# Kernel tuning notes

Measured on AMD Instinct MI355X. Metric: run time of the kernel, lower is better.

Reference implementation:

```python
import jax, jax.numpy as jnp
import numpy as np

N_NODES = 50000
N_EDGES = 800000
BATCH = 8
IN_CH = 64
OUT_CH = 64
K = 6


def setup_inputs() -> dict:
    key = jax.random.key(0)
    k1, k2, k3, k4 = jax.random.split(key, 4)
    x = jax.random.normal(k1, (BATCH, N_NODES, IN_CH), dtype=jnp.float32)
    edge_index = jax.random.randint(k2, (2, N_EDGES), 0, N_NODES, dtype=jnp.int64)
    # small weights keep the order-K Chebyshev recursion numerically stable
    edge_weight = jax.random.normal(k3, (N_EDGES,), dtype=jnp.float32) * 0.05
    W = jax.random.normal(k4, (K, IN_CH, OUT_CH), dtype=jnp.float32) * (1.0 / np.sqrt(IN_CH))
    bias = jnp.zeros((OUT_CH,), dtype=jnp.float32)
    return {"x": x, "edge_index": edge_index, "edge_weight": edge_weight, "W": W, "bias": bias}


def _spmm(edge_index, edge_weight, x, n_nodes):
    # sparse Laplacian @ x for batched features x: [B, N, C]
    src = edge_index[1]  # gather column
    dst = edge_index[0]  # scatter row
    msg = x[:, src, :] * edge_weight[None, :, None]      # [B, E, C]
    agg = jax.ops.segment_sum(msg.transpose(1, 0, 2), dst, num_segments=n_nodes)  # [N, B, C]
    return agg.transpose(1, 0, 2)                        # [B, N, C]


def reference(x, edge_index, edge_weight, W, bias):
    n = x.shape[1]
    t_prev = x                                            # T_0
    out = jnp.einsum('bnc,co->bno', t_prev, W[0])
    if K > 1:
        t_cur = _spmm(edge_index, edge_weight, x, n)      # T_1 = L x
        out = out + jnp.einsum('bnc,co->bno', t_cur, W[1])
        for k in range(2, K):
            t_next = 2.0 * _spmm(edge_index, edge_weight, t_cur, n) - t_prev
            out = out + jnp.einsum('bnc,co->bno', t_next, W[k])
            t_prev, t_cur = t_cur, t_next
    out = out + bias
    return out
```

## Files before the change

kernel.cpp:

```cpp
#include <hip/hip_runtime.h>

#define N_NODES 50000
#define N_EDGES 800000
#define BATCH 8
#define CH 64
#define BC (BATCH * CH)
#define WSZ (CH * CH)
#define NROWS (BATCH * N_NODES)
#define TELEMS ((size_t)NROWS * CH)
#define HIST_BLOCKS ((N_EDGES + 255) / 256)
#define CAST_BLOCKS ((int)(TELEMS / 4 / 256))
#define PACK_BLOCKS 12

typedef unsigned short u16;
typedef short bf16x8 __attribute__((ext_vector_type(8)));
typedef float f32x4 __attribute__((ext_vector_type(4)));
typedef unsigned short u16x4 __attribute__((ext_vector_type(4)));
typedef unsigned short u16x8 __attribute__((ext_vector_type(8)));

__device__ __forceinline__ u16 f2bf(float f) {
    unsigned x = __float_as_uint(f);
    return (u16)((x + 0x7fffu + ((x >> 16) & 1u)) >> 16);
}
__device__ __forceinline__ float b2f(u16 u) {
    return __uint_as_float(((unsigned)u) << 16);
}


__global__ __launch_bounds__(256) void hist_cast_kernel(
        const int* __restrict__ dst, int* __restrict__ cursor,
        const float* __restrict__ x, u16* __restrict__ xb) {
    int bid = blockIdx.x;
    if (bid < HIST_BLOCKS) {
        int e = bid * 256 + threadIdx.x;
        if (e < N_EDGES) atomicAdd(&cursor[dst[e]], 1);
        return;
    }
    size_t i = (size_t)(bid - HIST_BLOCKS) * 256 + threadIdx.x;
    f32x4 v = __builtin_nontemporal_load((const f32x4*)(x + i * 4));
    int c4 = (int)(i & 15);
    size_t bn = i >> 4;
    int b = (int)(bn / N_NODES);
    int n = (int)(bn - (size_t)b * N_NODES);
    u16x4 o;
    o.x = f2bf(v.x); o.y = f2bf(v.y); o.z = f2bf(v.z); o.w = f2bf(v.w);
    *(u16x4*)(xb + ((size_t)n * BATCH + b) * CH + c4 * 4) = o;
}

__global__ void scan_kernel(int* cursor, int* __restrict__ row_ptr, int n) {
    const int T = 1024;
    int tid = threadIdx.x;
    int per = (n + T - 1) / T;
    int s = tid * per;
    int e = s + per; if (e > n) e = n;
    int sum = 0;
    for (int i = s; i < e; ++i) sum += cursor[i];
    __shared__ int lds[1024];
    lds[tid] = sum;
    __syncthreads();
    for (int off = 1; off < 1024; off <<= 1) {
        int t = (tid >= off) ? lds[tid - off] : 0;
        __syncthreads();
        lds[tid] += t;
        __syncthreads();
    }
    int run = lds[tid] - sum;
    for (int i = s; i < e; ++i) {
        int v = cursor[i];
        row_ptr[i] = run;
        cursor[i]  = run;
        run += v;
    }
    if (tid == T - 1) row_ptr[n] = run;
}

__global__ __launch_bounds__(256) void scatter_pack_kernel(
        const int* __restrict__ dst, const int* __restrict__ src,
        const float* __restrict__ w, int* cursor, int2* __restrict__ edges,
        const float* __restrict__ W, u16* __restrict__ wpack) {
    int bid = blockIdx.x;
    if (bid < HIST_BLOCKS) {
        int e = bid * 256 + threadIdx.x;
        if (e >= N_EDGES) return;
        int d = dst[e];
        int p = atomicAdd(&cursor[d], 1);
        edges[p] = make_int2(src[e], __float_as_int(w[e]));
        return;
    }
    int id = (bid - HIST_BLOCKS) * 256 + threadIdx.x;
    if (id >= 48 * 64) return;
    int lane = id & 63, frag = id >> 6;
    int ct = frag & 3, cct = (frag >> 2) & 1, k = frag >> 3;
    int m = lane & 15, quad = lane >> 4;
    int c = ct * 16 + m;
#pragma unroll
    for (int j = 0; j < 8; ++j) {
        int cc = cct * 32 + quad * 8 + j;
        wpack[(size_t)id * 8 + j] = f2bf(W[k * WSZ + cc * CH + c]);
    }
}

template <bool HAS_PREV>
__global__ __launch_bounds__(256) void spmm_kernel(
        const u16* __restrict__ tcur,
        const u16* __restrict__ tprev,
        u16* __restrict__ tnext,
        const int* __restrict__ row_ptr,
        const int2* __restrict__ edges,
        int half) {
    const int node = blockIdx.x * 4 + (threadIdx.x >> 6);
    const int lane = threadIdx.x & 63;
    const size_t lo = (size_t)half * 256 + (size_t)lane * 4;

    float acc[4];
#pragma unroll
    for (int q = 0; q < 4; ++q) acc[q] = 0.f;

    const int beg = row_ptr[node], end = row_ptr[node + 1];
    for (int e0 = beg; e0 < end; e0 += 64) {
        int m = end - e0; if (m > 64) m = 64;
        int2 ev = edges[e0 + (lane < m ? lane : 0)];
        int j = 0;
        for (; j + 4 <= m; j += 4) {
            int   s0 = __shfl(ev.x, j);
            int   s1 = __shfl(ev.x, j + 1);
            int   s2 = __shfl(ev.x, j + 2);
            int   s3 = __shfl(ev.x, j + 3);
            float w0 = __int_as_float(__shfl(ev.y, j));
            float w1 = __int_as_float(__shfl(ev.y, j + 1));
            float w2 = __int_as_float(__shfl(ev.y, j + 2));
            float w3 = __int_as_float(__shfl(ev.y, j + 3));
            u16x4 v0 = *(const u16x4*)(tcur + (size_t)s0 * BC + lo);
            u16x4 v1 = *(const u16x4*)(tcur + (size_t)s1 * BC + lo);
            u16x4 v2 = *(const u16x4*)(tcur + (size_t)s2 * BC + lo);
            u16x4 v3 = *(const u16x4*)(tcur + (size_t)s3 * BC + lo);
#pragma unroll
            for (int q = 0; q < 4; ++q) acc[q] = fmaf(w0, b2f(v0[q]), acc[q]);
#pragma unroll
            for (int q = 0; q < 4; ++q) acc[q] = fmaf(w1, b2f(v1[q]), acc[q]);
#pragma unroll
            for (int q = 0; q < 4; ++q) acc[q] = fmaf(w2, b2f(v2[q]), acc[q]);
#pragma unroll
            for (int q = 0; q < 4; ++q) acc[q] = fmaf(w3, b2f(v3[q]), acc[q]);
        }
        for (; j < m; ++j) {
            int   s = __shfl(ev.x, j);
            float w = __int_as_float(__shfl(ev.y, j));
            u16x4 v = *(const u16x4*)(tcur + (size_t)s * BC + lo);
#pragma unroll
            for (int q = 0; q < 4; ++q) acc[q] = fmaf(w, b2f(v[q]), acc[q]);
        }
    }

    const size_t idx = (size_t)node * BC + lo;
    u16x4 o;
    if (HAS_PREV) {
        u16x4 pv = *(const u16x4*)(tprev + idx);
#pragma unroll
        for (int q = 0; q < 4; ++q) o[q] = f2bf(2.f * acc[q] - b2f(pv[q]));
    } else {
#pragma unroll
        for (int q = 0; q < 4; ++q) o[q] = f2bf(acc[q]);
    }
    *(u16x4*)(tnext + idx) = o;
}

template <int NK, bool ACCUM>
__global__ __launch_bounds__(256) void out_gemm(
        const u16* __restrict__ tbase, size_t tstride,
        const u16* __restrict__ wpack,
        const float* __restrict__ bias,
        float* __restrict__ out) {
    const int wave = threadIdx.x >> 6, lane = threadIdx.x & 63;
    const int tile = blockIdx.x * 4 + wave;
    const int row0 = tile * 16;
    const int m = lane & 15, quad = lane >> 4;

    bf16x8 A[NK][2];
#pragma unroll
    for (int k = 0; k < NK; ++k) {
        const u16* t = tbase + (size_t)k * tstride + (size_t)(row0 + m) * CH + quad * 8;
#pragma unroll
        for (int cct = 0; cct < 2; ++cct)
            A[k][cct] = *(const bf16x8*)(t + cct * 32);
    }

    f32x4 acc[4];
#pragma unroll
    for (int ct = 0; ct < 4; ++ct) acc[ct] = (f32x4){0.f, 0.f, 0.f, 0.f};

#pragma unroll
    for (int k = 0; k < NK; ++k) {
#pragma unroll
        for (int cct = 0; cct < 2; ++cct) {
#pragma unroll
            for (int ct = 0; ct < 4; ++ct) {
                bf16x8 B = *(const bf16x8*)(wpack + (size_t)(((k * 2 + cct) * 4 + ct) * 64 + lane) * 8);
                acc[ct] = __builtin_amdgcn_mfma_f32_16x16x32_bf16(A[k][cct], B, acc[ct], 0, 0, 0);
            }
        }
    }

#pragma unroll
    for (int ct = 0; ct < 4; ++ct) {
        const int c = ct * 16 + m;
        const float bv = bias[c];
#pragma unroll
        for (int r = 0; r < 4; ++r) {
            int row = row0 + quad * 4 + r;
            float* op = out + ((size_t)(row & 7) * N_NODES + (row >> 3)) * CH + c;
            float v = acc[ct][r];
            if (ACCUM) v += __builtin_nontemporal_load(op);
            else       v += bv;
            __builtin_nontemporal_store(v, op);
        }
    }
}

extern "C" void kernel_launch(void* const* d_in, const int* in_sizes, int n_in,
                              void* d_out, int out_size, void* d_ws, size_t ws_size,
                              hipStream_t stream) {
    const float* x    = (const float*)d_in[0];
    const int*   ei   = (const int*)d_in[1];
    const float* ew   = (const float*)d_in[2];
    const float* W    = (const float*)d_in[3];
    const float* bias = (const float*)d_in[4];
    float* out = (float*)d_out;

    const int* dst = ei;
    const int* src = ei + N_EDGES;

    const size_t SB = TELEMS * sizeof(u16);
    const size_t EXTRA = 2 * 200192 + (size_t)N_EDGES * sizeof(int2) + 49664;
    const size_t NEED_PRIMARY = 6 * SB + EXTRA;
    const bool primary = (ws_size >= NEED_PRIMARY);
    const int nbuf = primary ? 6 : 3;

    char* ws = (char*)d_ws;
    size_t off = 0;
    u16* tbase = (u16*)(ws + off); off += (size_t)nbuf * SB;
    int* row_ptr = (int*)(ws + off); off += 200192;
    int* cursor  = (int*)(ws + off); off += 200192;
    int2* edges  = (int2*)(ws + off); off += (size_t)N_EDGES * sizeof(int2);
    u16* wpack   = (u16*)(ws + off); off += 49664;
    (void)off; (void)n_in; (void)in_sizes; (void)out_size;

    (void)hipMemsetAsync(cursor, 0, (size_t)N_NODES * sizeof(int), stream);
    hist_cast_kernel<<<HIST_BLOCKS + CAST_BLOCKS, 256, 0, stream>>>(dst, cursor, x, tbase);
    scan_kernel<<<1, 1024, 0, stream>>>(cursor, row_ptr, N_NODES);
    scatter_pack_kernel<<<HIST_BLOCKS + PACK_BLOCKS, 256, 0, stream>>>(dst, src, ew, cursor,
                                                                       edges, W, wpack);

    const int SPMM_GRID = N_NODES / 4;
    const int GG = NROWS / 16 / 4;
    u16* t0 = tbase;
    if (primary) {
        u16* t1 = tbase + 1 * TELEMS;
        u16* t2 = tbase + 2 * TELEMS;
        u16* t3 = tbase + 3 * TELEMS;
        u16* t4 = tbase + 4 * TELEMS;
        u16* t5 = tbase + 5 * TELEMS;
        for (int h = 0; h < 2; ++h) {
            spmm_kernel<false><<<SPMM_GRID, 256, 0, stream>>>(t0, nullptr, t1, row_ptr, edges, h);
            spmm_kernel<true ><<<SPMM_GRID, 256, 0, stream>>>(t1, t0, t2, row_ptr, edges, h);
            spmm_kernel<true ><<<SPMM_GRID, 256, 0, stream>>>(t2, t1, t3, row_ptr, edges, h);
            spmm_kernel<true ><<<SPMM_GRID, 256, 0, stream>>>(t3, t2, t4, row_ptr, edges, h);
            spmm_kernel<true ><<<SPMM_GRID, 256, 0, stream>>>(t4, t3, t5, row_ptr, edges, h);
        }
        out_gemm<6, false><<<GG, 256, 0, stream>>>(tbase, TELEMS, wpack, bias, out);
    } else {
        u16* t1 = tbase + 1 * TELEMS;
        u16* t2 = tbase + 2 * TELEMS;
        spmm_kernel<false><<<SPMM_GRID, 256, 0, stream>>>(t0, nullptr, t1, row_ptr, edges, 0);
        spmm_kernel<false><<<SPMM_GRID, 256, 0, stream>>>(t0, nullptr, t1, row_ptr, edges, 1);
        out_gemm<2, false><<<GG, 256, 0, stream>>>(t0, TELEMS, wpack, bias, out);
        spmm_kernel<true ><<<SPMM_GRID, 256, 0, stream>>>(t1, t0, t2, row_ptr, edges, 0);
        spmm_kernel<true ><<<SPMM_GRID, 256, 0, stream>>>(t1, t0, t2, row_ptr, edges, 1);
        out_gemm<1, true ><<<GG, 256, 0, stream>>>(t2, TELEMS, wpack + 2 * WSZ, bias, out);
        spmm_kernel<true ><<<SPMM_GRID, 256, 0, stream>>>(t2, t1, t0, row_ptr, edges, 0);
        spmm_kernel<true ><<<SPMM_GRID, 256, 0, stream>>>(t2, t1, t0, row_ptr, edges, 1);
        out_gemm<1, true ><<<GG, 256, 0, stream>>>(t0, TELEMS, wpack + 3 * WSZ, bias, out);
        spmm_kernel<true ><<<SPMM_GRID, 256, 0, stream>>>(t0, t2, t1, row_ptr, edges, 0);
        spmm_kernel<true ><<<SPMM_GRID, 256, 0, stream>>>(t0, t2, t1, row_ptr, edges, 1);
        out_gemm<1, true ><<<GG, 256, 0, stream>>>(t1, TELEMS, wpack + 4 * WSZ, bias, out);
        spmm_kernel<true ><<<SPMM_GRID, 256, 0, stream>>>(t1, t0, t2, row_ptr, edges, 0);
        spmm_kernel<true ><<<SPMM_GRID, 256, 0, stream>>>(t1, t0, t2, row_ptr, edges, 1);
        out_gemm<1, true ><<<GG, 256, 0, stream>>>(t2, TELEMS, wpack + 5 * WSZ, bias, out);
    }
}
```

Measured before the change: 1.016 ms.

## Stage out_gemm A tiles via LDS per batch so output stores coalesce

Reorganizes out_gemm so that each block handles 64 nodes of a single batch. The A operands are loaded with global_load_lds into XOR-swizzled shared memory, and the MFMAs read from LDS. Before this, each 16-row tile interleaved batches (row&7), so output stores hit 8 scattered batch planes. Now each wave writes contiguous node rows within one batch. The cost is a shared-memory allocation (48KB for NK=6), which lowers occupancy, plus a barrier and tail guards for the partial last chunk.

```diff
diff --git a/kernel.cpp b/kernel.cpp
--- a/kernel.cpp
+++ b/kernel.cpp
@@ -11,6 +11,8 @@
 #define HIST_BLOCKS ((N_EDGES + 255) / 256)
 #define CAST_BLOCKS ((int)(TELEMS / 4 / 256))
 #define PACK_BLOCKS 12
+#define NCHUNK ((N_NODES + 63) / 64)
+#define GG (NCHUNK * 8)
 
 typedef unsigned short u16;
 typedef short bf16x8 __attribute__((ext_vector_type(8)));
@@ -171,32 +173,43 @@
         const u16* __restrict__ wpack,
         const float* __restrict__ bias,
         float* __restrict__ out) {
-    const int wave = threadIdx.x >> 6, lane = threadIdx.x & 63;
-    const int tile = blockIdx.x * 4 + wave;
-    const int row0 = tile * 16;
+    __shared__ u16 smem[NK * 4096];
+    const int tid = threadIdx.x;
+    const int wave = tid >> 6, lane = tid & 63;
+    const int b  = blockIdx.x & 7;
+    const int n0 = (blockIdx.x >> 3) << 6;
+
+#pragma unroll
+    for (int rr = 0; rr < 2 * NK; ++rr) {
+        int r384 = rr * 32 + (tid >> 3);
+        int k = r384 >> 6;
+        int r = r384 & 63;
+        int n = n0 + r; if (n >= N_NODES) n = N_NODES - 1;
+        const u16* gsrc = tbase + (size_t)k * tstride
+                        + ((size_t)n * 8 + b) * CH
+                        + (size_t)(((tid & 7) ^ (r & 7)) * 8);
+        u16* ldst = &smem[rr * 2048 + wave * 512];
+        __builtin_amdgcn_global_load_lds(
+            (const __attribute__((address_space(1))) unsigned int*)gsrc,
+            (__attribute__((address_space(3))) unsigned int*)ldst, 16, 0, 0);
+    }
+    __syncthreads();
+
     const int m = lane & 15, quad = lane >> 4;
-
-    bf16x8 A[NK][2];
+    f32x4 acc[4];
+#pragma unroll
+    for (int ct = 0; ct < 4; ++ct) acc[ct] = (f32x4){0.f, 0.f, 0.f, 0.f};
+
 #pragma unroll
     for (int k = 0; k < NK; ++k) {
-        const u16* t = tbase + (size_t)k * tstride + (size_t)(row0 + m) * CH + quad * 8;
-#pragma unroll
-        for (int cct = 0; cct < 2; ++cct)
-            A[k][cct] = *(const bf16x8*)(t + cct * 32);
-    }
-
-    f32x4 acc[4];
-#pragma unroll
-    for (int ct = 0; ct < 4; ++ct) acc[ct] = (f32x4){0.f, 0.f, 0.f, 0.f};
-
-#pragma unroll
-    for (int k = 0; k < NK; ++k) {
 #pragma unroll
         for (int cct = 0; cct < 2; ++cct) {
+            bf16x8 A = *(const bf16x8*)&smem[(size_t)(k * 64 + wave * 16 + m) * 64
+                                             + (((cct * 4 + quad) ^ (m & 7)) * 8)];
 #pragma unroll
             for (int ct = 0; ct < 4; ++ct) {
                 bf16x8 B = *(const bf16x8*)(wpack + (size_t)(((k * 2 + cct) * 4 + ct) * 64 + lane) * 8);
-                acc[ct] = __builtin_amdgcn_mfma_f32_16x16x32_bf16(A[k][cct], B, acc[ct], 0, 0, 0);
+                acc[ct] = __builtin_amdgcn_mfma_f32_16x16x32_bf16(A, B, acc[ct], 0, 0, 0);
             }
         }
     }
@@ -207,12 +220,14 @@
         const float bv = bias[c];
 #pragma unroll
         for (int r = 0; r < 4; ++r) {
-            int row = row0 + quad * 4 + r;
-            float* op = out + ((size_t)(row & 7) * N_NODES + (row >> 3)) * CH + c;
-            float v = acc[ct][r];
-            if (ACCUM) v += __builtin_nontemporal_load(op);
-            else       v += bv;
-            __builtin_nontemporal_store(v, op);
+            int n = n0 + wave * 16 + quad * 4 + r;
+            if (n < N_NODES) {
+                float* op = out + ((size_t)b * N_NODES + n) * CH + c;
+                float v = acc[ct][r];
+                if (ACCUM) v += __builtin_nontemporal_load(op);
+                else       v += bv;
+                __builtin_nontemporal_store(v, op);
+            }
         }
     }
 }
@@ -252,7 +267,6 @@
                                                                        edges, W, wpack);
 
     const int SPMM_GRID = N_NODES / 4;
-    const int GG = NROWS / 16 / 4;
     u16* t0 = tbase;
     if (primary) {
         u16* t1 = tbase + 1 * TELEMS;
```

Measured after the change: 1.018 ms. Within noise of the previous version (+0.2%).
